# Kernel tuning notes

Measured on AMD Instinct MI355X. Metric: run time of the kernel, lower is better.

Reference implementation:

```python
import jax, jax.numpy as jnp
import numpy as np

B, C_IN, C_OUT, T, R, CO = 8, 64, 64, 32, 32, 32


def setup_inputs() -> dict:
    key = jax.random.key(0)
    ks = jax.random.split(key, 8)
    scale = 1.0 / np.sqrt(C_IN)  # nn.Linear default uniform(-1/sqrt(in), 1/sqrt(in))
    w = lambda k: jax.random.uniform(k, (C_OUT, C_IN), jnp.float32, -scale, scale)
    return {
        "x": jax.random.normal(ks[0], (B, C_IN, T, R, CO), jnp.float32),
        "w_self": w(ks[1]),
        "w_tp": w(ks[2]),
        "w_tm": w(ks[3]),
        "w_rp": w(ks[4]),
        "w_rm": w(ks[5]),
        "w_cp": w(ks[6]),
        "w_cm": w(ks[7]),
    }


def _proj(v, w):
    # v: [B, t, r, c, C_in], w: [C_out, C_in] (nn.Linear layout)
    return jnp.einsum('btrci,oi->btrco', v, w)


def _shift_pad(a, axis, front):
    # pad 1 slice at front (True) or back (False) along `axis` of a 5-D tensor
    pads = [(0, 0)] * 5
    pads[axis] = (1, 0) if front else (0, 1)
    return jnp.pad(a, pads)


def reference(x, w_self, w_tp, w_tm, w_rp, w_rm, w_cp, w_cm):
    xp = jnp.transpose(x, (0, 2, 3, 4, 1))  # [B, T, R, Co, C_in]
    out = _proj(xp, w_self)
    if xp.shape[1] > 1:
        out = out + _shift_pad(_proj(xp[:, :-1], w_tp), 1, True)
        out = out + _shift_pad(_proj(xp[:, 1:], w_tm), 1, False)
    if xp.shape[2] > 1:
        out = out + _shift_pad(_proj(xp[:, :, :-1], w_rp), 2, True)
        out = out + _shift_pad(_proj(xp[:, :, 1:], w_rm), 2, False)
    if xp.shape[3] > 1:
        out = out + _shift_pad(_proj(xp[:, :, :, :-1], w_cp), 3, True)
        out = out + _shift_pad(_proj(xp[:, :, :, 1:], w_cm), 3, False)
    return jnp.transpose(out, (0, 4, 1, 2, 3))  # [B, C_out, T, R, Co]
```

## Files before the change

kernel.cpp:

```cpp
#include <hip/hip_runtime.h>


#define SB 32768
#define CIN 64
#define COUT 64
#define NB 8

typedef short s16x8 __attribute__((ext_vector_type(8)));
typedef __bf16 bf16x8 __attribute__((ext_vector_type(8)));
typedef float f32x4 __attribute__((ext_vector_type(4)));

__device__ __forceinline__ unsigned short f2bf(float f) {
    unsigned u = __float_as_uint(f);
    u += 0x7FFFu + ((u >> 16) & 1u);
    return (unsigned short)(u >> 16);
}

__global__ __launch_bounds__(256) void prep_kernel(const float* __restrict__ x,
                            const float* __restrict__ w0, const float* __restrict__ w1,
                            const float* __restrict__ w2, const float* __restrict__ w3,
                            const float* __restrict__ w4, const float* __restrict__ w5,
                            const float* __restrict__ w6,
                            unsigned short* __restrict__ ws) {
    __shared__ uint4 lds[2048];
    int bid = blockIdx.x;
    int tid = threadIdx.x;
    if (bid < 1024) {
        int b = bid >> 7;
        int sblk = (bid & 127) << 8;
        const float* xp = x + ((size_t)b * CIN) * SB + sblk + tid;
        unsigned pack[32];
#pragma unroll
        for (int i = 0; i < 32; ++i) {
            float f0 = xp[(size_t)(2 * i) * SB];
            float f1 = xp[(size_t)(2 * i + 1) * SB];
            pack[i] = (unsigned)f2bf(f0) | ((unsigned)f2bf(f1) << 16);
        }
#pragma unroll
        for (int j = 0; j < 8; ++j)
            lds[tid * 8 + (j ^ (tid & 7))] =
                make_uint4(pack[4 * j], pack[4 * j + 1], pack[4 * j + 2], pack[4 * j + 3]);
        __syncthreads();
        uint4* dst = (uint4*)(ws + ((size_t)b * SB + sblk) * CIN);
#pragma unroll
        for (int k = 0; k < 8; ++k) {
            int q = k * 256 + tid;
            int row = q >> 3, j = q & 7;
            dst[q] = lds[row * 8 + (j ^ (row & 7))];
        }
    } else {
        int tap = bid - 1024;
        const float* w = (tap == 0) ? w0 : (tap == 1) ? w1 : (tap == 2) ? w2
                       : (tap == 3) ? w3 : (tap == 4) ? w4 : (tap == 5) ? w5 : w6;
        unsigned p[8];
#pragma unroll
        for (int j = 0; j < 8; ++j) {
            float f0 = w[tid * 16 + 2 * j];
            float f1 = w[tid * 16 + 2 * j + 1];
            p[j] = (unsigned)f2bf(f0) | ((unsigned)f2bf(f1) << 16);
        }
        unsigned short* dst = ws + (size_t)NB * SB * CIN + tap * 4096 + tid * 16;
        uint4* dp = (uint4*)dst;
        dp[0] = make_uint4(p[0], p[1], p[2], p[3]);
        dp[1] = make_uint4(p[4], p[5], p[6], p[7]);
    }
}

__global__ __launch_bounds__(256, 4) void gemm_kernel(const unsigned short* __restrict__ ws,
                                                      float* __restrict__ out) {
    __shared__ uint4 alds[2560];
    const unsigned short* xq = ws;
    const unsigned short* wq = ws + (size_t)NB * SB * CIN;

    int bid = blockIdx.x;
    int b = bid >> 7;
    int sblk = (bid & 127) << 8;
    int tid = threadIdx.x;

    const uint4* xu = (const uint4*)(xq + (size_t)b * SB * CIN);
#pragma unroll
    for (int k = 0; k < 10; ++k) {
        int q = k * 256 + tid;
        int row = q >> 3, j = q & 7;
        int s = sblk - 32 + row;
        s = max(0, min(SB - 1, s));
        alds[row * 8 + (j ^ (row & 7))] = xu[(size_t)s * 8 + j];
    }
    __syncthreads();

    int lane = tid & 63;
    int wv = tid >> 6;
    int lo = lane & 15;
    int quad = lane >> 4;
    int sbase = sblk + wv * 64;
    int t = sblk >> 10;

    f32x4 acc[4][4];
#pragma unroll
    for (int mt = 0; mt < 4; ++mt)
#pragma unroll
        for (int nt = 0; nt < 4; ++nt)
            acc[mt][nt] = (f32x4){0.f, 0.f, 0.f, 0.f};

    int r_m[4], c_m[4], rl[4];
#pragma unroll
    for (int mt = 0; mt < 4; ++mt) {
        int s = sbase + mt * 16 + lo;
        r_m[mt] = (s >> 5) & 31;
        c_m[mt] = s & 31;
        rl[mt] = s - sblk + 32;
    }

    auto load_b = [&](const unsigned short* wt, int ks, int nt) -> bf16x8 {
        const unsigned short* bp = wt + (nt * 16 + lo) * 64 + ks * 32 + quad * 8;
        return __builtin_bit_cast(bf16x8, *(const s16x8*)bp);
    };

    auto run_tap_lds = [&](int tap, int d, const bool ok[4]) {
        const unsigned short* wt = wq + tap * 4096;
#pragma unroll
        for (int ks = 0; ks < 2; ++ks) {
            bf16x8 bf[4];
#pragma unroll
            for (int nt = 0; nt < 4; ++nt) bf[nt] = load_b(wt, ks, nt);
            int j = ks * 4 + quad;
#pragma unroll
            for (int mt = 0; mt < 4; ++mt) {
                int row = rl[mt] + d;
                s16x8 raw = *((const s16x8*)alds + row * 8 + (j ^ (row & 7)));
                s16x8 zz = {0, 0, 0, 0, 0, 0, 0, 0};
                raw = ok[mt] ? raw : zz;
                bf16x8 af = __builtin_bit_cast(bf16x8, raw);
#pragma unroll
                for (int nt = 0; nt < 4; ++nt)
                    acc[mt][nt] = __builtin_amdgcn_mfma_f32_16x16x32_bf16(af, bf[nt], acc[mt][nt], 0, 0, 0);
            }
        }
    };

    auto run_tap_glb = [&](int tap, int d) {
        const unsigned short* wt = wq + tap * 4096;
#pragma unroll
        for (int ks = 0; ks < 2; ++ks) {
            bf16x8 bf[4];
#pragma unroll
            for (int nt = 0; nt < 4; ++nt) bf[nt] = load_b(wt, ks, nt);
#pragma unroll
            for (int mt = 0; mt < 4; ++mt) {
                int s = sbase + mt * 16 + lo + d;
                const unsigned short* ap = xq + ((size_t)b * SB + s) * CIN + ks * 32 + quad * 8;
                bf16x8 af = __builtin_bit_cast(bf16x8, *(const s16x8*)ap);
#pragma unroll
                for (int nt = 0; nt < 4; ++nt)
                    acc[mt][nt] = __builtin_amdgcn_mfma_f32_16x16x32_bf16(af, bf[nt], acc[mt][nt], 0, 0, 0);
            }
        }
    };

    {
        bool ok_all[4] = {true, true, true, true};
        run_tap_lds(0, 0, ok_all);
    }
    if (t > 0)  run_tap_glb(1, -1024);
    if (t < 31) run_tap_glb(2, 1024);
    {
        bool ok[4];
#pragma unroll
        for (int mt = 0; mt < 4; ++mt) ok[mt] = (r_m[mt] > 0);
        run_tap_lds(3, -32, ok);
#pragma unroll
        for (int mt = 0; mt < 4; ++mt) ok[mt] = (r_m[mt] < 31);
        run_tap_lds(4, 32, ok);
#pragma unroll
        for (int mt = 0; mt < 4; ++mt) ok[mt] = (c_m[mt] > 0);
        run_tap_lds(5, -1, ok);
#pragma unroll
        for (int mt = 0; mt < 4; ++mt) ok[mt] = (c_m[mt] < 31);
        run_tap_lds(6, 1, ok);
    }

#pragma unroll
    for (int mt = 0; mt < 4; ++mt) {
#pragma unroll
        for (int nt = 0; nt < 4; ++nt) {
            int o = nt * 16 + lo;
            size_t off = ((size_t)(b * COUT + o)) * SB + sbase + mt * 16 + quad * 4;
            *(f32x4*)(out + off) = acc[mt][nt];
        }
    }
}

__global__ void fallback_kernel(const float* __restrict__ x,
                                const float* __restrict__ w0, const float* __restrict__ w1,
                                const float* __restrict__ w2, const float* __restrict__ w3,
                                const float* __restrict__ w4, const float* __restrict__ w5,
                                const float* __restrict__ w6,
                                float* __restrict__ out) {
    int bid = blockIdx.x;
    int b = bid >> 11;
    int og = (bid >> 7) & 15;
    int sblk = (bid & 127) << 8;
    int tid = threadIdx.x;
    __shared__ float wl[7][4][64];
    const float* wp[7] = {w0, w1, w2, w3, w4, w5, w6};
    for (int k = tid; k < 7 * 4 * 64; k += 256) {
        int tap = k >> 8, oo = (k >> 6) & 3, i = k & 63;
        wl[tap][oo][i] = wp[tap][(og * 4 + oo) * 64 + i];
    }
    __syncthreads();
    int s = sblk + tid;
    int t = s >> 10, r = (s >> 5) & 31, c = s & 31;
    const float* xb = x + (size_t)b * CIN * SB + s;
    float a0 = 0, a1 = 0, a2 = 0, a3 = 0;
    for (int i = 0; i < 64; ++i) {
        const float* xi = xb + (size_t)i * SB;
        float vs = xi[0];
        float vtp = (t > 0) ? xi[-1024] : 0.f;
        float vtm = (t < 31) ? xi[1024] : 0.f;
        float vrp = (r > 0) ? xi[-32] : 0.f;
        float vrm = (r < 31) ? xi[32] : 0.f;
        float vcp = (c > 0) ? xi[-1] : 0.f;
        float vcm = (c < 31) ? xi[1] : 0.f;
        a0 += wl[0][0][i] * vs + wl[1][0][i] * vtp + wl[2][0][i] * vtm + wl[3][0][i] * vrp + wl[4][0][i] * vrm + wl[5][0][i] * vcp + wl[6][0][i] * vcm;
        a1 += wl[0][1][i] * vs + wl[1][1][i] * vtp + wl[2][1][i] * vtm + wl[3][1][i] * vrp + wl[4][1][i] * vrm + wl[5][1][i] * vcp + wl[6][1][i] * vcm;
        a2 += wl[0][2][i] * vs + wl[1][2][i] * vtp + wl[2][2][i] * vtm + wl[3][2][i] * vrp + wl[4][2][i] * vrm + wl[5][2][i] * vcp + wl[6][2][i] * vcm;
        a3 += wl[0][3][i] * vs + wl[1][3][i] * vtp + wl[2][3][i] * vtm + wl[3][3][i] * vrp + wl[4][3][i] * vrm + wl[5][3][i] * vcp + wl[6][3][i] * vcm;
    }
    size_t obase = ((size_t)b * COUT + og * 4) * SB + s;
    out[obase] = a0;
    out[obase + SB] = a1;
    out[obase + 2 * (size_t)SB] = a2;
    out[obase + 3 * (size_t)SB] = a3;
}

extern "C" void kernel_launch(void* const* d_in, const int* in_sizes, int n_in,
                              void* d_out, int out_size, void* d_ws, size_t ws_size,
                              hipStream_t stream) {
    const float* x = (const float*)d_in[0];
    const float* w0 = (const float*)d_in[1];
    const float* w1 = (const float*)d_in[2];
    const float* w2 = (const float*)d_in[3];
    const float* w3 = (const float*)d_in[4];
    const float* w4 = (const float*)d_in[5];
    const float* w5 = (const float*)d_in[6];
    const float* w6 = (const float*)d_in[7];
    float* out = (float*)d_out;

    size_t need = (size_t)NB * SB * CIN * 2 + (size_t)7 * 4096 * 2;
    if (d_ws != nullptr && ws_size >= need) {
        unsigned short* wsp = (unsigned short*)d_ws;
        prep_kernel<<<1031, 256, 0, stream>>>(x, w0, w1, w2, w3, w4, w5, w6, wsp);
        gemm_kernel<<<1024, 256, 0, stream>>>(wsp, out);
    } else {
        fallback_kernel<<<8 * 16 * 128, 256, 0, stream>>>(x, w0, w1, w2, w3, w4, w5, w6, out);
    }
}
```

Measured before the change: 175.9 us.

## Fuse x transpose/bf16 conversion into conv kernel, drop workspace round-trip

Removes the separate prep pass that transposed and converted the full x tensor to a bf16 channel-last workspace. The conv kernel now reads fp32 x directly, converts it to bf16 while filling its LDS tile with halo, and gathers the t±1 taps straight from fp32 global memory with on-the-fly conversion. A tiny kernel still converts the weights. This saves a full write and reread of the activation tensor. In exchange the t-neighbour taps do strided scalar fp32 loads, which may be less efficient than the old vectorised bf16 loads, and launch bounds drop the occupancy hint.

```diff
diff --git a/kernel.cpp b/kernel.cpp
--- a/kernel.cpp
+++ b/kernel.cpp
@@ -10,81 +10,70 @@
 typedef __bf16 bf16x8 __attribute__((ext_vector_type(8)));
 typedef float f32x4 __attribute__((ext_vector_type(4)));
 
-__device__ __forceinline__ unsigned short f2bf(float f) {
+__device__ __forceinline__ unsigned f2bf(float f) {
     unsigned u = __float_as_uint(f);
     u += 0x7FFFu + ((u >> 16) & 1u);
-    return (unsigned short)(u >> 16);
-}
-
-__global__ __launch_bounds__(256) void prep_kernel(const float* __restrict__ x,
-                            const float* __restrict__ w0, const float* __restrict__ w1,
-                            const float* __restrict__ w2, const float* __restrict__ w3,
-                            const float* __restrict__ w4, const float* __restrict__ w5,
-                            const float* __restrict__ w6,
+    return u >> 16;
+}
+__device__ __forceinline__ unsigned pk2(float lo, float hi) {
+    return f2bf(lo) | (f2bf(hi) << 16);
+}
+
+__global__ __launch_bounds__(256) void wprep_kernel(const float* __restrict__ w0,
+                            const float* __restrict__ w1, const float* __restrict__ w2,
+                            const float* __restrict__ w3, const float* __restrict__ w4,
+                            const float* __restrict__ w5, const float* __restrict__ w6,
                             unsigned short* __restrict__ ws) {
-    __shared__ uint4 lds[2048];
-    int bid = blockIdx.x;
+    int tap = blockIdx.x;
     int tid = threadIdx.x;
-    if (bid < 1024) {
-        int b = bid >> 7;
-        int sblk = (bid & 127) << 8;
-        const float* xp = x + ((size_t)b * CIN) * SB + sblk + tid;
-        unsigned pack[32];
-#pragma unroll
-        for (int i = 0; i < 32; ++i) {
-            float f0 = xp[(size_t)(2 * i) * SB];
-            float f1 = xp[(size_t)(2 * i + 1) * SB];
-            pack[i] = (unsigned)f2bf(f0) | ((unsigned)f2bf(f1) << 16);
-        }
-#pragma unroll
-        for (int j = 0; j < 8; ++j)
-            lds[tid * 8 + (j ^ (tid & 7))] =
-                make_uint4(pack[4 * j], pack[4 * j + 1], pack[4 * j + 2], pack[4 * j + 3]);
-        __syncthreads();
-        uint4* dst = (uint4*)(ws + ((size_t)b * SB + sblk) * CIN);
-#pragma unroll
-        for (int k = 0; k < 8; ++k) {
-            int q = k * 256 + tid;
-            int row = q >> 3, j = q & 7;
-            dst[q] = lds[row * 8 + (j ^ (row & 7))];
-        }
-    } else {
-        int tap = bid - 1024;
-        const float* w = (tap == 0) ? w0 : (tap == 1) ? w1 : (tap == 2) ? w2
-                       : (tap == 3) ? w3 : (tap == 4) ? w4 : (tap == 5) ? w5 : w6;
-        unsigned p[8];
-#pragma unroll
-        for (int j = 0; j < 8; ++j) {
-            float f0 = w[tid * 16 + 2 * j];
-            float f1 = w[tid * 16 + 2 * j + 1];
-            p[j] = (unsigned)f2bf(f0) | ((unsigned)f2bf(f1) << 16);
-        }
-        unsigned short* dst = ws + (size_t)NB * SB * CIN + tap * 4096 + tid * 16;
-        uint4* dp = (uint4*)dst;
-        dp[0] = make_uint4(p[0], p[1], p[2], p[3]);
-        dp[1] = make_uint4(p[4], p[5], p[6], p[7]);
-    }
-}
-
-__global__ __launch_bounds__(256, 4) void gemm_kernel(const unsigned short* __restrict__ ws,
-                                                      float* __restrict__ out) {
+    const float* w = (tap == 0) ? w0 : (tap == 1) ? w1 : (tap == 2) ? w2
+                   : (tap == 3) ? w3 : (tap == 4) ? w4 : (tap == 5) ? w5 : w6;
+    unsigned p[8];
+#pragma unroll
+    for (int j = 0; j < 8; ++j)
+        p[j] = pk2(w[tid * 16 + 2 * j], w[tid * 16 + 2 * j + 1]);
+    uint4* dp = (uint4*)(ws + tap * 4096 + tid * 16);
+    dp[0] = make_uint4(p[0], p[1], p[2], p[3]);
+    dp[1] = make_uint4(p[4], p[5], p[6], p[7]);
+}
+
+__global__ __launch_bounds__(256) void conv_kernel(const float* __restrict__ x,
+                                                   const unsigned short* __restrict__ wq,
+                                                   float* __restrict__ out) {
     __shared__ uint4 alds[2560];
-    const unsigned short* xq = ws;
-    const unsigned short* wq = ws + (size_t)NB * SB * CIN;
-
     int bid = blockIdx.x;
     int b = bid >> 7;
     int sblk = (bid & 127) << 8;
     int tid = threadIdx.x;
-
-    const uint4* xu = (const uint4*)(xq + (size_t)b * SB * CIN);
-#pragma unroll
-    for (int k = 0; k < 10; ++k) {
-        int q = k * 256 + tid;
-        int row = q >> 3, j = q & 7;
-        int s = sblk - 32 + row;
+    const float* xb = x + (size_t)b * CIN * SB;
+
+    {
+        int rl = 32 + tid;
+        const float* xp = xb + sblk + tid;
+#pragma unroll
+        for (int c = 0; c < 4; ++c) {
+            unsigned pk[8];
+#pragma unroll
+            for (int u = 0; u < 8; ++u)
+                pk[u] = pk2(xp[(size_t)(c * 16 + 2 * u) * SB],
+                            xp[(size_t)(c * 16 + 2 * u + 1) * SB]);
+            alds[rl * 8 + ((2 * c) ^ (rl & 7))] = make_uint4(pk[0], pk[1], pk[2], pk[3]);
+            alds[rl * 8 + ((2 * c + 1) ^ (rl & 7))] = make_uint4(pk[4], pk[5], pk[6], pk[7]);
+        }
+    }
+    {
+        int hrow = tid & 63;
+        int rl = (hrow < 32) ? hrow : hrow + 256;
+        int s = sblk - 32 + rl;
         s = max(0, min(SB - 1, s));
-        alds[row * 8 + (j ^ (row & 7))] = xu[(size_t)s * 8 + j];
+        int ic = tid >> 6;
+        const float* xp = xb + s + (size_t)(ic * 16) * SB;
+        unsigned pk[8];
+#pragma unroll
+        for (int u = 0; u < 8; ++u)
+            pk[u] = pk2(xp[(size_t)(2 * u) * SB], xp[(size_t)(2 * u + 1) * SB]);
+        alds[rl * 8 + ((2 * ic) ^ (rl & 7))] = make_uint4(pk[0], pk[1], pk[2], pk[3]);
+        alds[rl * 8 + ((2 * ic + 1) ^ (rl & 7))] = make_uint4(pk[4], pk[5], pk[6], pk[7]);
     }
     __syncthreads();
 
@@ -138,18 +127,23 @@
         }
     };
 
-    auto run_tap_glb = [&](int tap, int d) {
+    auto run_tap_gather = [&](int tap, int d) {
         const unsigned short* wt = wq + tap * 4096;
 #pragma unroll
         for (int ks = 0; ks < 2; ++ks) {
             bf16x8 bf[4];
 #pragma unroll
             for (int nt = 0; nt < 4; ++nt) bf[nt] = load_b(wt, ks, nt);
+            const float* gp = xb + (size_t)(ks * 32 + quad * 8) * SB + d;
 #pragma unroll
             for (int mt = 0; mt < 4; ++mt) {
-                int s = sbase + mt * 16 + lo + d;
-                const unsigned short* ap = xq + ((size_t)b * SB + s) * CIN + ks * 32 + quad * 8;
-                bf16x8 af = __builtin_bit_cast(bf16x8, *(const s16x8*)ap);
+                const float* ap = gp + sbase + mt * 16 + lo;
+                unsigned pk[4];
+#pragma unroll
+                for (int u = 0; u < 4; ++u)
+                    pk[u] = pk2(ap[(size_t)(2 * u) * SB], ap[(size_t)(2 * u + 1) * SB]);
+                uint4 v = make_uint4(pk[0], pk[1], pk[2], pk[3]);
+                bf16x8 af = __builtin_bit_cast(bf16x8, v);
 #pragma unroll
                 for (int nt = 0; nt < 4; ++nt)
                     acc[mt][nt] = __builtin_amdgcn_mfma_f32_16x16x32_bf16(af, bf[nt], acc[mt][nt], 0, 0, 0);
@@ -161,8 +155,8 @@
         bool ok_all[4] = {true, true, true, true};
         run_tap_lds(0, 0, ok_all);
     }
-    if (t > 0)  run_tap_glb(1, -1024);
-    if (t < 31) run_tap_glb(2, 1024);
+    if (t > 0)  run_tap_gather(1, -1024);
+    if (t < 31) run_tap_gather(2, 1024);
     {
         bool ok[4];
 #pragma unroll
@@ -246,11 +240,11 @@
     const float* w6 = (const float*)d_in[7];
     float* out = (float*)d_out;
 
-    size_t need = (size_t)NB * SB * CIN * 2 + (size_t)7 * 4096 * 2;
+    size_t need = (size_t)7 * 4096 * 2;
     if (d_ws != nullptr && ws_size >= need) {
         unsigned short* wsp = (unsigned short*)d_ws;
-        prep_kernel<<<1031, 256, 0, stream>>>(x, w0, w1, w2, w3, w4, w5, w6, wsp);
-        gemm_kernel<<<1024, 256, 0, stream>>>(wsp, out);
+        wprep_kernel<<<7, 256, 0, stream>>>(w0, w1, w2, w3, w4, w5, w6, wsp);
+        conv_kernel<<<1024, 256, 0, stream>>>(x, wsp, out);
     } else {
         fallback_kernel<<<8 * 16 * 128, 256, 0, stream>>>(x, w0, w1, w2, w3, w4, w5, w6, out);
     }
```

After: 159.0 us. 1.11x faster.
